# Kernel tuning notes

Measured on AMD Instinct MI355X. Metric: run time of the kernel, lower is better.

## Reference

```python
import jax, jax.numpy as jnp
import numpy as np

N_HEADS = 16
N_KV_HEADS = 4
HEAD_DIM = 128


def apply_rope(x, cos, sin):
    # x: [b, h, s, head_dim]; cos/sin: [1, 1, s, head_dim//2]
    d = x.shape[-1] // 2
    x1, x2 = x[..., :d], x[..., d:]
    return jnp.concatenate([x1 * cos - x2 * sin, x1 * sin + x2 * cos], axis=-1)


def setup_inputs() -> dict:
    key = jax.random.key(0)
    ks = jax.random.split(key, 9)
    b, s, dim = 2, 2048, 2048
    inp = {
        "x": jax.random.normal(ks[0], (b, s, dim), jnp.float32),
        "cos": jax.random.normal(ks[1], (1, 1, s, HEAD_DIM // 2), jnp.float32),
        "sin": jax.random.normal(ks[2], (1, 1, s, HEAD_DIM // 2), jnp.float32),
        "Wq": jax.random.normal(ks[3], (dim, N_HEADS * HEAD_DIM), jnp.float32) * 0.02,
        "bq": jax.random.normal(ks[4], (N_HEADS * HEAD_DIM,), jnp.float32) * 0.02,
        "Wkv": jax.random.normal(ks[5], (dim, 2 * N_KV_HEADS * HEAD_DIM), jnp.float32) * 0.02,
        "bkv": jax.random.normal(ks[6], (2 * N_KV_HEADS * HEAD_DIM,), jnp.float32) * 0.02,
        "Wo": jax.random.normal(ks[7], (N_HEADS * HEAD_DIM, dim), jnp.float32) * 0.02,
        "bo": jax.random.normal(ks[8], (dim,), jnp.float32) * 0.02,
        "causal": 1,
    }
    return inp


def reference(x, cos, sin, Wq, bq, Wkv, bkv, Wo, bo, causal):
    b, s, dim = x.shape
    scale = 1.0 / np.sqrt(HEAD_DIM)
    # QKV projections (torch Linear with weight stored transposed here)
    q = (x @ Wq + bq).reshape(b, s, N_HEADS, HEAD_DIM).transpose(0, 2, 1, 3)
    kv = x @ Wkv + bkv  # [b, s, 2*n_kv*hd]
    k, v = jnp.split(kv, 2, axis=-1)
    k = k.reshape(b, s, N_KV_HEADS, HEAD_DIM).transpose(0, 2, 1, 3)
    v = v.reshape(b, s, N_KV_HEADS, HEAD_DIM).transpose(0, 2, 1, 3)
    q = apply_rope(q, cos, sin)
    k = apply_rope(k, cos, sin)
    # GQA: repeat kv heads
    rep = N_HEADS // N_KV_HEADS
    k = jnp.repeat(k, rep, axis=1)
    v = jnp.repeat(v, rep, axis=1)
    logits = jnp.einsum("bhqd,bhkd->bhqk", q, k) * scale
    if causal:
        mask = jnp.tril(jnp.ones((s, s), dtype=bool))
        logits = jnp.where(mask[None, None], logits, jnp.finfo(logits.dtype).min)
    scores = jax.nn.softmax(logits, axis=-1)
    vo = jnp.einsum("bhqk,bhkd->bhqd", scores, v)
    vo = vo.transpose(0, 2, 1, 3).reshape(b, s, N_HEADS * HEAD_DIM)
    out = vo @ Wo + bo
    return out
```

## Files before the change

kernel.cpp:

```cpp
#include <hip/hip_runtime.h>
#include <hip/hip_bf16.h>

typedef __bf16 bf16x8 __attribute__((ext_vector_type(8)));
typedef float  f32x4  __attribute__((ext_vector_type(4)));
typedef unsigned int u32;

#define GLD_LDS16(gp, lp) __builtin_amdgcn_global_load_lds( \
    (const __attribute__((address_space(1))) u32*)(gp), \
    (__attribute__((address_space(3))) u32*)(lp), 16, 0, 0)

template<int CTRL>
__device__ __forceinline__ float dpp_rot(float x) {
    int y = __builtin_amdgcn_update_dpp(__float_as_int(x), __float_as_int(x),
                                        CTRL, 0xF, 0xF, false);
    return __int_as_float(y);
}
__device__ __forceinline__ float rowmax16(float x) {
    x = fmaxf(x, dpp_rot<0x121>(x));
    x = fmaxf(x, dpp_rot<0x122>(x));
    x = fmaxf(x, dpp_rot<0x124>(x));
    x = fmaxf(x, dpp_rot<0x128>(x));
    return x;
}
__device__ __forceinline__ float rowsum16(float x) {
    x += dpp_rot<0x121>(x);
    x += dpp_rot<0x122>(x);
    x += dpp_rot<0x124>(x);
    x += dpp_rot<0x128>(x);
    return x;
}


__global__ __launch_bounds__(256) void f32_to_bf16_kernel(
    const float* __restrict__ in, __bf16* __restrict__ out, size_t n) {
    size_t i = ((size_t)blockIdx.x * 256 + threadIdx.x) * 8;
    if (i >= n) return;
    float4 a = *(const float4*)(in + i);
    float4 b = *(const float4*)(in + i + 4);
    bf16x8 v;
    v[0] = (__bf16)a.x; v[1] = (__bf16)a.y; v[2] = (__bf16)a.z; v[3] = (__bf16)a.w;
    v[4] = (__bf16)b.x; v[5] = (__bf16)b.y; v[6] = (__bf16)b.z; v[7] = (__bf16)b.w;
    *(bf16x8*)(out + i) = v;
}

__global__ __launch_bounds__(256) void transpose_to_bf16_kernel(
    const float* __restrict__ W, __bf16* __restrict__ Wt, int K, int N) {
    __shared__ float tile[32][33];
    int n0 = blockIdx.x * 32, k0 = blockIdx.y * 32;
    int tx = threadIdx.x, ty = threadIdx.y;
    #pragma unroll
    for (int i = 0; i < 32; i += 8)
        tile[ty + i][tx] = W[(size_t)(k0 + ty + i) * N + n0 + tx];
    __syncthreads();
    #pragma unroll
    for (int i = 0; i < 32; i += 8)
        Wt[(size_t)(n0 + ty + i) * K + k0 + tx] = (__bf16)tile[tx][ty + i];
}

__global__ __launch_bounds__(256) void concat_bias_kernel(
    const float* __restrict__ bq, const float* __restrict__ bkv,
    float* __restrict__ bqkv) {
    int i = blockIdx.x * 256 + threadIdx.x;
    if (i < 2048) bqkv[i] = bq[i];
    else if (i < 3072) bqkv[i] = bkv[i - 2048];
}

__global__ __launch_bounds__(256) void transpose_v_kernel(
    const __bf16* __restrict__ qkv, __bf16* __restrict__ vtg, int S) {
    __shared__ __bf16 tile[32][33];
    int s0 = blockIdx.x * 32, d0 = blockIdx.y * 32, z = blockIdx.z;
    int b = z >> 2, kvh = z & 3;
    int tx = threadIdx.x, ty = threadIdx.y;
    #pragma unroll
    for (int i = 0; i < 32; i += 8)
        tile[ty + i][tx] =
            qkv[((size_t)b * S + s0 + ty + i) * 3072 + 2560 + kvh * 128 + d0 + tx];
    __syncthreads();
    #pragma unroll
    for (int i = 0; i < 32; i += 8)
        vtg[((size_t)z * 128 + d0 + ty + i) * S + s0 + tx] = tile[tx][ty + i];
}

#define BM 128
#define BN 128
#define BK 64

template <typename OutT>
__global__ __launch_bounds__(256) void gemm_bt_bias_kernel(
    const __bf16* __restrict__ A, const __bf16* __restrict__ Bt,
    const float* __restrict__ bias, OutT* __restrict__ C,
    int M, int N, int K) {
    __shared__ __bf16 As[BM * BK];
    __shared__ __bf16 Bs[BN * BK];
    int tid  = threadIdx.x;
    int bm   = blockIdx.x;
    int bn   = blockIdx.y;
    int wave = tid >> 6;
    int lane = tid & 63;
    int wm   = (wave >> 1) * 64;
    int wn   = (wave & 1) * 64;
    int quad = lane >> 4;
    int l16  = lane & 15;
    int gr   = wave * 32 + (lane >> 3);
    int gc   = (lane & 7) * 8;

    f32x4 acc[4][4];
    f32x4 zero = {0.f, 0.f, 0.f, 0.f};
    #pragma unroll
    for (int i = 0; i < 4; ++i)
        #pragma unroll
        for (int j = 0; j < 4; ++j) acc[i][j] = zero;

    const __bf16* Abase = A  + (size_t)(bm * BM) * K;
    const __bf16* Bbase = Bt + (size_t)(bn * BN) * K;

    for (int k0 = 0; k0 < K; k0 += BK) {
        if (k0) __syncthreads();
        #pragma unroll
        for (int i = 0; i < 4; ++i) {
            GLD_LDS16(Abase + (size_t)(gr + i * 8) * K + k0 + gc,
                      &As[(wave * 32 + i * 8) * BK]);
            GLD_LDS16(Bbase + (size_t)(gr + i * 8) * K + k0 + gc,
                      &Bs[(wave * 32 + i * 8) * BK]);
        }
        __syncthreads();

        bf16x8 af[4][2], bf[4][2];
        #pragma unroll
        for (int i = 0; i < 4; ++i)
            #pragma unroll
            for (int kc = 0; kc < 2; ++kc)
                af[i][kc] = *(bf16x8*)&As[(wm + i * 16 + l16) * BK + kc * 32 + quad * 8];
        #pragma unroll
        for (int j = 0; j < 4; ++j)
            #pragma unroll
            for (int kc = 0; kc < 2; ++kc)
                bf[j][kc] = *(bf16x8*)&Bs[(wn + j * 16 + l16) * BK + kc * 32 + quad * 8];
        #pragma unroll
        for (int kc = 0; kc < 2; ++kc)
            #pragma unroll
            for (int i = 0; i < 4; ++i)
                #pragma unroll
                for (int j = 0; j < 4; ++j)
                    acc[i][j] = __builtin_amdgcn_mfma_f32_16x16x32_bf16(
                        af[i][kc], bf[j][kc], acc[i][j], 0, 0, 0);
    }

    #pragma unroll
    for (int i = 0; i < 4; ++i) {
        int row = bm * BM + wm + i * 16 + quad * 4;
        #pragma unroll
        for (int j = 0; j < 4; ++j) {
            int col  = bn * BN + wn + j * 16 + l16;
            float bv = bias[col];
            #pragma unroll
            for (int r = 0; r < 4; ++r)
                C[(size_t)(row + r) * N + col] = (OutT)(acc[i][j][r] + bv);
        }
    }
}

__global__ __launch_bounds__(256) void rope_kernel(
    __bf16* __restrict__ buf, const float* __restrict__ cosp,
    const float* __restrict__ sinp, int heads, int rowstride, int coloff,
    int S, int total) {
    int idx = blockIdx.x * 256 + threadIdx.x;
    if (idx >= total) return;
    int d  = idx & 63;
    int t2 = idx >> 6;
    int h  = t2 % heads;
    int r  = t2 / heads;
    int s  = r & (S - 1);
    size_t base = (size_t)r * rowstride + coloff + h * 128;
    float x1 = (float)buf[base + d];
    float x2 = (float)buf[base + d + 64];
    float c  = cosp[s * 64 + d];
    float sn = sinp[s * 64 + d];
    buf[base + d]      = (__bf16)(x1 * c - x2 * sn);
    buf[base + d + 64] = (__bf16)(x1 * sn + x2 * c);
}

#define PS_STR 72

__global__ __launch_bounds__(256, 2) void flash_mfma_kernel(
    const __bf16* __restrict__ qkv,
    const __bf16* __restrict__ vtg,
    __bf16* __restrict__ vo,
    const int* __restrict__ causal_p, int S) {
    __shared__ __bf16 Ks[2][64 * 128];
    __shared__ __bf16 Ps[4 * 16 * PS_STR];

    const int QKV = 3072;
    int tid  = threadIdx.x;
    int wave = tid >> 6;
    int lane = tid & 63;
    int quad = lane >> 4;
    int l16  = lane & 15;
    int id   = blockIdx.x;
    int xcd  = id & 7;
    int b    = xcd >> 2;
    int kvh  = xcd & 3;
    int rest = id >> 3;
    int hh   = rest & 3;
    int pair = rest >> 2;
    int h    = kvh * 4 + hh;
    int causal = causal_p[0];
    const float SCALE = 0.08838834764831845f;

    const __bf16* vB = vtg + ((size_t)(b * 4 + kvh) * 128) * S;

    #pragma unroll 1
    for (int phase = 0; phase < 2; ++phase) {
        int qt = phase ? (31 - pair) : pair;
        int q0 = qt * 64;
        int nt = causal ? (qt + 1) : (S / 64);

        bf16x8 a_frag[4];
        size_t qrow = ((size_t)b * S + q0 + wave * 16 + l16) * QKV + h * 128 + quad * 8;
        #pragma unroll
        for (int kc = 0; kc < 4; ++kc)
            a_frag[kc] = *(const bf16x8*)(qkv + qrow + kc * 32);

        f32x4 o_acc[8];
        f32x4 zero4 = {0.f, 0.f, 0.f, 0.f};
        #pragma unroll
        for (int dt = 0; dt < 8; ++dt) o_acc[dt] = zero4;
        float m_[4], l_[4];
        #pragma unroll
        for (int r = 0; r < 4; ++r) { m_[r] = -1e30f; l_[r] = 0.f; }
        int qrow_d = q0 + wave * 16 + quad * 4;

        __syncthreads();
        {
            size_t kg = ((size_t)b * S + wave * 16 + l16) * QKV + 2048 + kvh * 128 + quad * 8;
            #pragma unroll
            for (int kc = 0; kc < 4; ++kc)
                GLD_LDS16(qkv + kg + kc * 32, &Ks[0][(wave * 4 + kc) * 512]);
        }

        for (int t = 0; t < nt; ++t) {
            int cur = t & 1;
            __syncthreads();
            if (t + 1 < nt) {
                size_t kg = ((size_t)b * S + (t + 1) * 64 + wave * 16 + l16) * QKV
                            + 2048 + kvh * 128 + quad * 8;
                #pragma unroll
                for (int kc = 0; kc < 4; ++kc)
                    GLD_LDS16(qkv + kg + kc * 32, &Ks[1 - cur][(wave * 4 + kc) * 512]);
            }
            int j0 = t * 64;

            bf16x8 vf[8][2];
            #pragma unroll
            for (int dt = 0; dt < 8; ++dt) {
                const __bf16* vp = vB + (size_t)(dt * 16 + l16) * S + j0 + quad * 8;
                vf[dt][0] = *(const bf16x8*)(vp);
                vf[dt][1] = *(const bf16x8*)(vp + 32);
            }

            f32x4 s_t[4];
            #pragma unroll
            for (int jt = 0; jt < 4; ++jt) s_t[jt] = zero4;
            #pragma unroll
            for (int jt = 0; jt < 4; ++jt)
                #pragma unroll
                for (int kc = 0; kc < 4; ++kc) {
                    bf16x8 kf = *(bf16x8*)&Ks[cur][(jt * 4 + kc) * 512 + lane * 8];
                    s_t[jt] = __builtin_amdgcn_mfma_f32_16x16x32_bf16(
                        a_frag[kc], kf, s_t[jt], 0, 0, 0);
                }

            int diag = causal && (t == nt - 1);
            #pragma unroll
            for (int jt = 0; jt < 4; ++jt)
                #pragma unroll
                for (int r = 0; r < 4; ++r) {
                    float sv = s_t[jt][r] * SCALE;
                    if (diag && (j0 + jt * 16 + l16 > qrow_d + r)) sv = -1e30f;
                    s_t[jt][r] = sv;
                }

            float alpha[4];
            #pragma unroll
            for (int r = 0; r < 4; ++r) {
                float v = fmaxf(fmaxf(s_t[0][r], s_t[1][r]),
                                fmaxf(s_t[2][r], s_t[3][r]));
                v = rowmax16(v);
                float m_new = fmaxf(m_[r], v);
                alpha[r] = __expf(m_[r] - m_new);
                m_[r] = m_new;
                float rs = 0.f;
                #pragma unroll
                for (int jt = 0; jt < 4; ++jt) {
                    float p = __expf(s_t[jt][r] - m_new);
                    s_t[jt][r] = p;
                    rs += p;
                }
                l_[r] = l_[r] * alpha[r] + rs;
            }
            #pragma unroll
            for (int jt = 0; jt < 4; ++jt)
                #pragma unroll
                for (int r = 0; r < 4; ++r)
                    Ps[(wave * 16 + quad * 4 + r) * PS_STR + jt * 16 + l16] =
                        (__bf16)s_t[jt][r];
            #pragma unroll
            for (int dt = 0; dt < 8; ++dt)
                #pragma unroll
                for (int r = 0; r < 4; ++r) o_acc[dt][r] *= alpha[r];

            bf16x8 p0 = *(bf16x8*)&Ps[(wave * 16 + l16) * PS_STR + quad * 8];
            bf16x8 p1 = *(bf16x8*)&Ps[(wave * 16 + l16) * PS_STR + 32 + quad * 8];
            #pragma unroll
            for (int dt = 0; dt < 8; ++dt) {
                o_acc[dt] = __builtin_amdgcn_mfma_f32_16x16x32_bf16(
                    p0, vf[dt][0], o_acc[dt], 0, 0, 0);
                o_acc[dt] = __builtin_amdgcn_mfma_f32_16x16x32_bf16(
                    p1, vf[dt][1], o_acc[dt], 0, 0, 0);
            }
        }

        float invl[4];
        #pragma unroll
        for (int r = 0; r < 4; ++r) invl[r] = 1.f / rowsum16(l_[r]);
        size_t obase = ((size_t)b * S + q0 + wave * 16 + quad * 4) * 2048
                       + h * 128 + l16;
        #pragma unroll
        for (int dt = 0; dt < 8; ++dt)
            #pragma unroll
            for (int r = 0; r < 4; ++r)
                vo[obase + (size_t)r * 2048 + dt * 16] = (__bf16)(o_acc[dt][r] * invl[r]);
    }
}


extern "C" void kernel_launch(void* const* d_in, const int* in_sizes, int n_in,
                              void* d_out, int out_size, void* d_ws, size_t ws_size,
                              hipStream_t stream) {
    const float* x    = (const float*)d_in[0];
    const float* cosp = (const float*)d_in[1];
    const float* sinp = (const float*)d_in[2];
    const float* Wq   = (const float*)d_in[3];
    const float* bq   = (const float*)d_in[4];
    const float* Wkv  = (const float*)d_in[5];
    const float* bkv  = (const float*)d_in[6];
    const float* Wo   = (const float*)d_in[7];
    const float* bo   = (const float*)d_in[8];
    const int* causal = (const int*)d_in[9];
    float* out = (float*)d_out;

    const int B = 2, S = 2048;
    const int M = B * S;

    char* w = (char*)d_ws;
    __bf16* x16    = (__bf16*)w; w += (size_t)M * 2048 * 2;
    __bf16* Wqkvt  = (__bf16*)w; w += (size_t)3072 * 2048 * 2;
    __bf16* Wot    = (__bf16*)w; w += (size_t)2048 * 2048 * 2;
    float*  bqkv   = (float*)w;  w += (size_t)3072 * 4;
    __bf16* qkvbuf = (__bf16*)w; w += (size_t)M * 3072 * 2;
    __bf16* vobuf  = x16;
    __bf16* vtg    = Wqkvt;

    f32_to_bf16_kernel<<<(M * 2048) / (256 * 8), 256, 0, stream>>>(x, x16, (size_t)M * 2048);
    transpose_to_bf16_kernel<<<dim3(2048 / 32, 2048 / 32), dim3(32, 8), 0, stream>>>(Wq, Wqkvt, 2048, 2048);
    transpose_to_bf16_kernel<<<dim3(1024 / 32, 2048 / 32), dim3(32, 8), 0, stream>>>(Wkv, Wqkvt + (size_t)2048 * 2048, 2048, 1024);
    transpose_to_bf16_kernel<<<dim3(2048 / 32, 2048 / 32), dim3(32, 8), 0, stream>>>(Wo, Wot, 2048, 2048);
    concat_bias_kernel<<<12, 256, 0, stream>>>(bq, bkv, bqkv);
    gemm_bt_bias_kernel<__bf16><<<dim3(M / BM, 3072 / BN), 256, 0, stream>>>(x16, Wqkvt, bqkv, qkvbuf, M, 3072, 2048);
    {
        int totq = M * 16 * 64;
        rope_kernel<<<(totq + 255) / 256, 256, 0, stream>>>(qkvbuf, cosp, sinp, 16, 3072, 0, S, totq);
        int totk = M * 4 * 64;
        rope_kernel<<<(totk + 255) / 256, 256, 0, stream>>>(qkvbuf, cosp, sinp, 4, 3072, 2048, S, totk);
    }
    transpose_v_kernel<<<dim3(S / 32, 128 / 32, B * 4), dim3(32, 8), 0, stream>>>(qkvbuf, vtg, S);
    flash_mfma_kernel<<<dim3(512), 256, 0, stream>>>(qkvbuf, vtg, vobuf, causal, S);
    gemm_bt_bias_kernel<float><<<dim3(M / BM, 2048 / BN), 256, 0, stream>>>(vobuf, Wot, bo, out, M, 2048, 2048);
}
```

Before: 431.5 us.

## Use 128-row query tiles with 8 waves in flash kernel and fuse RoPE launches

The attention kernel now runs 512 threads per block, each covering one 128-row query tile, instead of processing two balanced 64-row tiles per block. The shared K tile is reused across 8 waves, and blocks are ordered heaviest-first to replace the explicit pairing for load balance. The causal mask is applied on the last two key tiles, and the P staging stride changes. The separate Q and K RoPE launches are merged into a single kernel covering all 20 head slots.

New measurement: 488.2 us. +13.1%, slower.

```diff
diff --git a/kernel.cpp b/kernel.cpp
--- a/kernel.cpp
+++ b/kernel.cpp
@@ -162,16 +162,16 @@
 
 __global__ __launch_bounds__(256) void rope_kernel(
     __bf16* __restrict__ buf, const float* __restrict__ cosp,
-    const float* __restrict__ sinp, int heads, int rowstride, int coloff,
-    int S, int total) {
+    const float* __restrict__ sinp, int S, int total) {
     int idx = blockIdx.x * 256 + threadIdx.x;
     if (idx >= total) return;
-    int d  = idx & 63;
-    int t2 = idx >> 6;
-    int h  = t2 % heads;
-    int r  = t2 / heads;
-    int s  = r & (S - 1);
-    size_t base = (size_t)r * rowstride + coloff + h * 128;
+    int d    = idx & 63;
+    int t2   = idx >> 6;
+    int slot = t2 % 20;
+    int r    = t2 / 20;
+    int s    = r & (S - 1);
+    int coloff = (slot < 16) ? slot * 128 : 2048 + (slot - 16) * 128;
+    size_t base = (size_t)r * 3072 + coloff;
     float x1 = (float)buf[base + d];
     float x2 = (float)buf[base + d + 64];
     float c  = cosp[s * 64 + d];
@@ -180,15 +180,15 @@
     buf[base + d + 64] = (__bf16)(x1 * sn + x2 * c);
 }
 
-#define PS_STR 72
-
-__global__ __launch_bounds__(256, 2) void flash_mfma_kernel(
+#define PS_STR 68
+
+__global__ __launch_bounds__(512, 4) void flash_mfma_kernel(
     const __bf16* __restrict__ qkv,
     const __bf16* __restrict__ vtg,
     __bf16* __restrict__ vo,
     const int* __restrict__ causal_p, int S) {
     __shared__ __bf16 Ks[2][64 * 128];
-    __shared__ __bf16 Ps[4 * 16 * PS_STR];
+    __shared__ __bf16 Ps[8 * 16 * PS_STR];
 
     const int QKV = 3072;
     int tid  = threadIdx.x;
@@ -202,135 +202,134 @@
     int kvh  = xcd & 3;
     int rest = id >> 3;
     int hh   = rest & 3;
-    int pair = rest >> 2;
+    int qt   = 15 - (rest >> 2);
     int h    = kvh * 4 + hh;
+    int q0   = qt * 128;
     int causal = causal_p[0];
     const float SCALE = 0.08838834764831845f;
 
     const __bf16* vB = vtg + ((size_t)(b * 4 + kvh) * 128) * S;
-
-    #pragma unroll 1
-    for (int phase = 0; phase < 2; ++phase) {
-        int qt = phase ? (31 - pair) : pair;
-        int q0 = qt * 64;
-        int nt = causal ? (qt + 1) : (S / 64);
-
-        bf16x8 a_frag[4];
+    int nt = causal ? (2 * qt + 2) : (S / 64);
+
+    bf16x8 a_frag[4];
+    {
         size_t qrow = ((size_t)b * S + q0 + wave * 16 + l16) * QKV + h * 128 + quad * 8;
         #pragma unroll
         for (int kc = 0; kc < 4; ++kc)
             a_frag[kc] = *(const bf16x8*)(qkv + qrow + kc * 32);
-
-        f32x4 o_acc[8];
-        f32x4 zero4 = {0.f, 0.f, 0.f, 0.f};
-        #pragma unroll
-        for (int dt = 0; dt < 8; ++dt) o_acc[dt] = zero4;
-        float m_[4], l_[4];
-        #pragma unroll
-        for (int r = 0; r < 4; ++r) { m_[r] = -1e30f; l_[r] = 0.f; }
-        int qrow_d = q0 + wave * 16 + quad * 4;
-
+    }
+
+    f32x4 o_acc[8];
+    f32x4 zero4 = {0.f, 0.f, 0.f, 0.f};
+    #pragma unroll
+    for (int dt = 0; dt < 8; ++dt) o_acc[dt] = zero4;
+    float m_[4], l_[4];
+    #pragma unroll
+    for (int r = 0; r < 4; ++r) { m_[r] = -1e30f; l_[r] = 0.f; }
+    int qrow_d = q0 + wave * 16 + quad * 4;
+
+    #pragma unroll
+    for (int i = 0; i < 2; ++i) {
+        int c = wave * 2 + i;
+        size_t kg = ((size_t)b * S + (c >> 2) * 16 + l16) * QKV
+                    + 2048 + kvh * 128 + (c & 3) * 32 + quad * 8;
+        GLD_LDS16(qkv + kg, &Ks[0][c * 512]);
+    }
+
+    for (int t = 0; t < nt; ++t) {
+        int cur = t & 1;
         __syncthreads();
-        {
-            size_t kg = ((size_t)b * S + wave * 16 + l16) * QKV + 2048 + kvh * 128 + quad * 8;
-            #pragma unroll
-            for (int kc = 0; kc < 4; ++kc)
-                GLD_LDS16(qkv + kg + kc * 32, &Ks[0][(wave * 4 + kc) * 512]);
-        }
-
-        for (int t = 0; t < nt; ++t) {
-            int cur = t & 1;
-            __syncthreads();
-            if (t + 1 < nt) {
-                size_t kg = ((size_t)b * S + (t + 1) * 64 + wave * 16 + l16) * QKV
-                            + 2048 + kvh * 128 + quad * 8;
-                #pragma unroll
-                for (int kc = 0; kc < 4; ++kc)
-                    GLD_LDS16(qkv + kg + kc * 32, &Ks[1 - cur][(wave * 4 + kc) * 512]);
+        if (t + 1 < nt) {
+            #pragma unroll
+            for (int i = 0; i < 2; ++i) {
+                int c = wave * 2 + i;
+                size_t kg = ((size_t)b * S + (t + 1) * 64 + (c >> 2) * 16 + l16) * QKV
+                            + 2048 + kvh * 128 + (c & 3) * 32 + quad * 8;
+                GLD_LDS16(qkv + kg, &Ks[1 - cur][c * 512]);
             }
-            int j0 = t * 64;
-
-            bf16x8 vf[8][2];
-            #pragma unroll
-            for (int dt = 0; dt < 8; ++dt) {
-                const __bf16* vp = vB + (size_t)(dt * 16 + l16) * S + j0 + quad * 8;
-                vf[dt][0] = *(const bf16x8*)(vp);
-                vf[dt][1] = *(const bf16x8*)(vp + 32);
+        }
+        int j0 = t * 64;
+
+        bf16x8 vf[8][2];
+        #pragma unroll
+        for (int dt = 0; dt < 8; ++dt) {
+            const __bf16* vp = vB + (size_t)(dt * 16 + l16) * S + j0 + quad * 8;
+            vf[dt][0] = *(const bf16x8*)(vp);
+            vf[dt][1] = *(const bf16x8*)(vp + 32);
+        }
+
+        f32x4 s_t[4];
+        #pragma unroll
+        for (int jt = 0; jt < 4; ++jt) s_t[jt] = zero4;
+        #pragma unroll
+        for (int jt = 0; jt < 4; ++jt)
+            #pragma unroll
+            for (int kc = 0; kc < 4; ++kc) {
+                bf16x8 kf = *(bf16x8*)&Ks[cur][(jt * 4 + kc) * 512 + lane * 8];
+                s_t[jt] = __builtin_amdgcn_mfma_f32_16x16x32_bf16(
+                    a_frag[kc], kf, s_t[jt], 0, 0, 0);
             }
 
-            f32x4 s_t[4];
-            #pragma unroll
-            for (int jt = 0; jt < 4; ++jt) s_t[jt] = zero4;
-            #pragma unroll
-            for (int jt = 0; jt < 4; ++jt)
-                #pragma unroll
-                for (int kc = 0; kc < 4; ++kc) {
-                    bf16x8 kf = *(bf16x8*)&Ks[cur][(jt * 4 + kc) * 512 + lane * 8];
-                    s_t[jt] = __builtin_amdgcn_mfma_f32_16x16x32_bf16(
-                        a_frag[kc], kf, s_t[jt], 0, 0, 0);
-                }
-
-            int diag = causal && (t == nt - 1);
-            #pragma unroll
-            for (int jt = 0; jt < 4; ++jt)
-                #pragma unroll
-                for (int r = 0; r < 4; ++r) {
-                    float sv = s_t[jt][r] * SCALE;
-                    if (diag && (j0 + jt * 16 + l16 > qrow_d + r)) sv = -1e30f;
-                    s_t[jt][r] = sv;
-                }
-
-            float alpha[4];
+        int diag = causal && (t >= nt - 2);
+        #pragma unroll
+        for (int jt = 0; jt < 4; ++jt)
             #pragma unroll
             for (int r = 0; r < 4; ++r) {
-                float v = fmaxf(fmaxf(s_t[0][r], s_t[1][r]),
-                                fmaxf(s_t[2][r], s_t[3][r]));
-                v = rowmax16(v);
-                float m_new = fmaxf(m_[r], v);
-                alpha[r] = __expf(m_[r] - m_new);
-                m_[r] = m_new;
-                float rs = 0.f;
-                #pragma unroll
-                for (int jt = 0; jt < 4; ++jt) {
-                    float p = __expf(s_t[jt][r] - m_new);
-                    s_t[jt][r] = p;
-                    rs += p;
-                }
-                l_[r] = l_[r] * alpha[r] + rs;
+                float sv = s_t[jt][r] * SCALE;
+                if (diag && (j0 + jt * 16 + l16 > qrow_d + r)) sv = -1e30f;
+                s_t[jt][r] = sv;
             }
-            #pragma unroll
-            for (int jt = 0; jt < 4; ++jt)
-                #pragma unroll
-                for (int r = 0; r < 4; ++r)
-                    Ps[(wave * 16 + quad * 4 + r) * PS_STR + jt * 16 + l16] =
-                        (__bf16)s_t[jt][r];
-            #pragma unroll
-            for (int dt = 0; dt < 8; ++dt)
-                #pragma unroll
-                for (int r = 0; r < 4; ++r) o_acc[dt][r] *= alpha[r];
-
-            bf16x8 p0 = *(bf16x8*)&Ps[(wave * 16 + l16) * PS_STR + quad * 8];
-            bf16x8 p1 = *(bf16x8*)&Ps[(wave * 16 + l16) * PS_STR + 32 + quad * 8];
-            #pragma unroll
-            for (int dt = 0; dt < 8; ++dt) {
-                o_acc[dt] = __builtin_amdgcn_mfma_f32_16x16x32_bf16(
-                    p0, vf[dt][0], o_acc[dt], 0, 0, 0);
-                o_acc[dt] = __builtin_amdgcn_mfma_f32_16x16x32_bf16(
-                    p1, vf[dt][1], o_acc[dt], 0, 0, 0);
+
+        float alpha[4];
+        #pragma unroll
+        for (int r = 0; r < 4; ++r) {
+            float v = fmaxf(fmaxf(s_t[0][r], s_t[1][r]),
+                            fmaxf(s_t[2][r], s_t[3][r]));
+            v = rowmax16(v);
+            float m_new = fmaxf(m_[r], v);
+            alpha[r] = __expf(m_[r] - m_new);
+            m_[r] = m_new;
+            float rs = 0.f;
+            #pragma unroll
+            for (int jt = 0; jt < 4; ++jt) {
+                float p = __expf(s_t[jt][r] - m_new);
+                s_t[jt][r] = p;
+                rs += p;
             }
-        }
-
-        float invl[4];
-        #pragma unroll
-        for (int r = 0; r < 4; ++r) invl[r] = 1.f / rowsum16(l_[r]);
-        size_t obase = ((size_t)b * S + q0 + wave * 16 + quad * 4) * 2048
-                       + h * 128 + l16;
+            l_[r] = l_[r] * alpha[r] + rs;
+        }
+        #pragma unroll
+        for (int jt = 0; jt < 4; ++jt)
+            #pragma unroll
+            for (int r = 0; r < 4; ++r)
+                Ps[(wave * 16 + quad * 4 + r) * PS_STR + jt * 16 + l16] =
+                    (__bf16)s_t[jt][r];
         #pragma unroll
         for (int dt = 0; dt < 8; ++dt)
             #pragma unroll
-            for (int r = 0; r < 4; ++r)
-                vo[obase + (size_t)r * 2048 + dt * 16] = (__bf16)(o_acc[dt][r] * invl[r]);
-    }
+            for (int r = 0; r < 4; ++r) o_acc[dt][r] *= alpha[r];
+
+        bf16x8 p0 = *(bf16x8*)&Ps[(wave * 16 + l16) * PS_STR + quad * 8];
+        bf16x8 p1 = *(bf16x8*)&Ps[(wave * 16 + l16) * PS_STR + 32 + quad * 8];
+        #pragma unroll
+        for (int dt = 0; dt < 8; ++dt) {
+            o_acc[dt] = __builtin_amdgcn_mfma_f32_16x16x32_bf16(
+                p0, vf[dt][0], o_acc[dt], 0, 0, 0);
+            o_acc[dt] = __builtin_amdgcn_mfma_f32_16x16x32_bf16(
+                p1, vf[dt][1], o_acc[dt], 0, 0, 0);
+        }
+    }
+
+    float invl[4];
+    #pragma unroll
+    for (int r = 0; r < 4; ++r) invl[r] = 1.f / rowsum16(l_[r]);
+    size_t obase = ((size_t)b * S + q0 + wave * 16 + quad * 4) * 2048
+                   + h * 128 + l16;
+    #pragma unroll
+    for (int dt = 0; dt < 8; ++dt)
+        #pragma unroll
+        for (int r = 0; r < 4; ++r)
+            vo[obase + (size_t)r * 2048 + dt * 16] = (__bf16)(o_acc[dt][r] * invl[r]);
 }
 
 
@@ -368,12 +367,10 @@
     concat_bias_kernel<<<12, 256, 0, stream>>>(bq, bkv, bqkv);
     gemm_bt_bias_kernel<__bf16><<<dim3(M / BM, 3072 / BN), 256, 0, stream>>>(x16, Wqkvt, bqkv, qkvbuf, M, 3072, 2048);
     {
-        int totq = M * 16 * 64;
-        rope_kernel<<<(totq + 255) / 256, 256, 0, stream>>>(qkvbuf, cosp, sinp, 16, 3072, 0, S, totq);
-        int totk = M * 4 * 64;
-        rope_kernel<<<(totk + 255) / 256, 256, 0, stream>>>(qkvbuf, cosp, sinp, 4, 3072, 2048, S, totk);
+        int tot = M * 20 * 64;
+        rope_kernel<<<(tot + 255) / 256, 256, 0, stream>>>(qkvbuf, cosp, sinp, S, tot);
     }
     transpose_v_kernel<<<dim3(S / 32, 128 / 32, B * 4), dim3(32, 8), 0, stream>>>(qkvbuf, vtg, S);
-    flash_mfma_kernel<<<dim3(512), 256, 0, stream>>>(qkvbuf, vtg, vobuf, causal, S);
+    flash_mfma_kernel<<<dim3(512), 512, 0, stream>>>(qkvbuf, vtg, vobuf, causal, S);
     gemm_bt_bias_kernel<float><<<dim3(M / BM, 2048 / BN), 256, 0, stream>>>(vobuf, Wot, bo, out, M, 2048, 2048);
 }
```
